# Performance work log

Measured on AMD Instinct MI355X. Metric: run time of the kernel, lower is better.

Reference implementation:

```python
import jax, jax.numpy as jnp
import numpy as np

H = 128; D = 16; L = 4
NP_ = 50000; NL_ = 10000; EPP = 500000; ELP = 100000; EPL = 100000


def _rbf(d):
    # GaussianSmearing(start=0, stop=8, num_gaussians=16)
    off = jnp.linspace(0.0, 8.0, D)
    coeff = -0.5 / ((8.0 / (D - 1)) ** 2)
    x = d[:, None] - off[None, :]
    return jnp.exp(coeff * x * x)


def _layer_norm(x, w, b, eps=1e-5):
    mu = jnp.mean(x, axis=-1, keepdims=True)
    var = jnp.var(x, axis=-1, keepdims=True)
    return (x - mu) * jax.lax.rsqrt(var + eps) * w + b


def _block(x_src, x_dst, src, dst, ea, Wf_, bf_, Ws_, bs_, bnw, bnb, lnw, lnb):
    # CGConv message: z = [x_i(dst), x_j(src), edge_attr]
    z = jnp.concatenate([x_dst[dst], x_src[src], ea], axis=-1)  # [E, 2H+D]
    m = jax.nn.sigmoid(z @ Wf_ + bf_) * jax.nn.softplus(z @ Ws_ + bs_)
    agg = jax.ops.segment_sum(m, dst, num_segments=x_dst.shape[0])
    # BatchNorm1d in eval mode with running_mean=0, running_var=1
    agg = agg * (bnw / jnp.sqrt(1.0 + 1e-5)) + bnb
    out = agg + x_dst            # CGConv internal residual
    out = _layer_norm(out, lnw, lnb)
    out = jax.nn.relu(out)
    return out + x_dst           # ResidualCGConvBlock residual (dropout=identity in eval)


def setup_inputs() -> dict:
    key = jax.random.key(0)
    ks = jax.random.split(key, 16)
    s = lambda n: 1.0 / np.sqrt(n)
    inp = {
        'x_protein': jax.random.normal(ks[0], (NP_, 6), jnp.float32),
        'x_ligand': jax.random.normal(ks[1], (NL_, 6), jnp.float32),
        'ei_pp': jnp.stack([jax.random.randint(ks[2], (EPP,), 0, NP_),
                            jax.random.randint(ks[3], (EPP,), 0, NP_)]).astype(jnp.int32),
        'ea_pp': jax.random.uniform(ks[4], (EPP,), jnp.float32, 0.0, 8.0),
        'ei_lp': jnp.stack([jax.random.randint(ks[5], (ELP,), 0, NL_),
                            jax.random.randint(ks[6], (ELP,), 0, NP_)]).astype(jnp.int32),
        'ea_lp': jax.random.uniform(ks[7], (ELP,), jnp.float32, 0.0, 8.0),
        'ei_pl': jnp.stack([jax.random.randint(ks[8], (EPL,), 0, NP_),
                            jax.random.randint(ks[9], (EPL,), 0, NL_)]).astype(jnp.int32),
        'ea_pl': jax.random.uniform(ks[10], (EPL,), jnp.float32, 0.0, 8.0),
        'Wp': jax.random.normal(ks[11], (6, H), jnp.float32) * s(6),
        'bp': jnp.zeros((H,), jnp.float32),
        'Wl': jax.random.normal(ks[12], (6, H), jnp.float32) * s(6),
        'bl': jnp.zeros((H,), jnp.float32),
        'Wf': jax.random.normal(ks[13], (L, 3, 2 * H + D, H), jnp.float32) * s(2 * H + D),
        'bf': jnp.zeros((L, 3, H), jnp.float32),
        'Ws': jax.random.normal(ks[14], (L, 3, 2 * H + D, H), jnp.float32) * s(2 * H + D),
        'bs': jnp.zeros((L, 3, H), jnp.float32),
        'bn_w': jnp.ones((L, 3, H), jnp.float32),
        'bn_b': jnp.zeros((L, 3, H), jnp.float32),
        'ln_w': jnp.ones((L, 3, H), jnp.float32),
        'ln_b': jnp.zeros((L, 3, H), jnp.float32),
        'lno_w': jnp.ones((H,), jnp.float32),
        'lno_b': jnp.zeros((H,), jnp.float32),
        'fc_w': jax.random.normal(ks[15], (H, 21), jnp.float32) * s(H),
        'fc_b': jnp.zeros((21,), jnp.float32),
    }
    return inp


def reference(x_protein, x_ligand, ei_pp, ea_pp, ei_lp, ea_lp, ei_pl, ea_pl,
              Wp, bp, Wl, bl, Wf, bf, Ws, bs, bn_w, bn_b, ln_w, ln_b,
              lno_w, lno_b, fc_w, fc_b):
    xp = x_protein @ Wp + bp
    xl = x_ligand @ Wl + bl
    rpp = _rbf(ea_pp); rlp = _rbf(ea_lp); rpl = _rbf(ea_pl)
    for l in range(L):
        # HeteroConv aggr='sum': protein receives from pp and lp; ligand from pl
        p_pp = _block(xp, xp, ei_pp[0], ei_pp[1], rpp, Wf[l, 0], bf[l, 0], Ws[l, 0], bs[l, 0],
                      bn_w[l, 0], bn_b[l, 0], ln_w[l, 0], ln_b[l, 0])
        p_lp = _block(xl, xp, ei_lp[0], ei_lp[1], rlp, Wf[l, 1], bf[l, 1], Ws[l, 1], bs[l, 1],
                      bn_w[l, 1], bn_b[l, 1], ln_w[l, 1], ln_b[l, 1])
        l_pl = _block(xp, xl, ei_pl[0], ei_pl[1], rpl, Wf[l, 2], bf[l, 2], Ws[l, 2], bs[l, 2],
                      bn_w[l, 2], bn_b[l, 2], ln_w[l, 2], ln_b[l, 2])
        xp, xl = p_pp + p_lp, l_pl
    out = _layer_norm(xp, lno_w, lno_b)
    return out @ fc_w + fc_b
```

## Files before the change

### kernel.cpp

```cpp
#include <hip/hip_runtime.h>
#include <hip/hip_bf16.h>
#include <math.h>

#define H 128

typedef __bf16 bf16x8 __attribute__((ext_vector_type(8)));
typedef float f32x4 __attribute__((ext_vector_type(4)));
typedef float f32x2 __attribute__((ext_vector_type(2)));
typedef __hip_bfloat16 bf16;
typedef unsigned int uint32;

static __device__ __forceinline__ float bf2f(bf16 v){ return __bfloat162float(v); }
static __device__ __forceinline__ bf16 f2bf(float v){ return __float2bfloat16(v); }
static __device__ __forceinline__ float u2f_lo(uint32 v){ return __uint_as_float(v << 16); }
static __device__ __forceinline__ float u2f_hi(uint32 v){ return __uint_as_float(v & 0xffff0000u); }

union bfpack { struct { bf16 lo, hi; } h; uint32 u; };
static __device__ __forceinline__ uint32 pack_bf2(float a, float b){
  bfpack p; p.h.lo = f2bf(a); p.h.hi = f2bf(b); return p.u;
}

static __device__ __forceinline__ int unperm64(int r){
  int base = r & ~63; int g = r & 63; int t = g >> 4; int j = g & 15;
  return base + 4*j + t;
}

#define NBIN 256
#define PREP_WP_N (4*1024*128)
#define PREP_WL_N (4*512*128)
#define RBF_N     (12*(NBIN+1)*128)

__global__ void prep_all(const float* __restrict__ Wf, const float* __restrict__ Ws,
                         const float* __restrict__ bfv, const float* __restrict__ bsv,
                         bf16* __restrict__ Wt_p, float* __restrict__ Bias_p,
                         bf16* __restrict__ Wt_l, float* __restrict__ Bias_l,
                         bf16* __restrict__ T2,
                         const float* __restrict__ Xp, const float* __restrict__ Wp,
                         const float* __restrict__ bp, float* __restrict__ Xpo,
                         bf16* __restrict__ Xpb, int NP,
                         const float* __restrict__ Xl, const float* __restrict__ Wl,
                         const float* __restrict__ bl, float* __restrict__ Xlo,
                         bf16* __restrict__ Xlb, int NL){
  int t = blockIdx.x*blockDim.x + threadIdx.x;
  if (t < PREP_WP_N){
    int k = t & 127; int idx = t >> 7;
    int rs = idx & 1023; int l = idx >> 10;
    int r = unperm64(rs);
    int rel, c, row0; const float* W; float bias = 0.f;
    if (r < 256)      { rel=0; c=r>>1;        row0=128; W = (r&1)?Ws:Wf; }
    else if (r < 512) { rel=2; c=(r-256)>>1;  row0=128; W = (r&1)?Ws:Wf; }
    else if (r < 640) { rel=0; c=r-512; row0=0; W=Wf; bias = bfv[(l*3+rel)*H+c]; }
    else if (r < 768) { rel=0; c=r-640; row0=0; W=Ws; bias = bsv[(l*3+rel)*H+c]; }
    else if (r < 896) { rel=1; c=r-768; row0=0; W=Wf; bias = bfv[(l*3+rel)*H+c]; }
    else              { rel=1; c=r-896; row0=0; W=Ws; bias = bsv[(l*3+rel)*H+c]; }
    Wt_p[t] = f2bf(W[((size_t)(l*3+rel)*272 + row0 + k)*H + c]);
    if (k == 0) Bias_p[l*1024 + r] = bias;
    return;
  }
  t -= PREP_WP_N;
  if (t < PREP_WL_N){
    int k = t & 127; int idx = t >> 7;
    int rs = idx & 511; int l = idx >> 9;
    int r = unperm64(rs);
    int rel, c, row0; const float* W; float bias = 0.f;
    if (r < 256)      { rel=1; c=r>>1;   row0=128; W = (r&1)?Ws:Wf; }
    else if (r < 384) { rel=2; c=r-256; row0=0; W=Wf; bias = bfv[(l*3+rel)*H+c]; }
    else              { rel=2; c=r-384; row0=0; W=Ws; bias = bsv[(l*3+rel)*H+c]; }
    Wt_l[t] = f2bf(W[((size_t)(l*3+rel)*272 + row0 + k)*H + c]);
    if (k == 0) Bias_l[l*512 + r] = bias;
    return;
  }
  t -= PREP_WL_N;
  if (t < RBF_N){
    int c = t & 127;
    int b = (t >> 7) % (NBIN+1);
    int pr = t / ((NBIN+1)*128);
    float d0 = (float)b * (8.0f/(float)NBIN);
    const float* wf = Wf + ((size_t)pr*272 + 256)*H + c;
    const float* ws = Ws + ((size_t)pr*272 + 256)*H + c;
    float f0=0.f, s0=0.f;
    #pragma unroll
    for (int k=0;k<16;k++){
      float o = 0.533333333f*(float)k;
      float tt = d0 - o;
      float r0 = __expf(-1.7578125f*tt*tt);
      f0 += r0*wf[(size_t)k*H]; s0 += r0*ws[(size_t)k*H];
    }
    bf16* o = T2 + ((size_t)(pr*(NBIN+1) + b))*256 + 2*c;
    o[0]=f2bf(f0); o[1]=f2bf(s0);
    return;
  }
  t -= RBF_N;
  {
    int idx = t;
    const float* Xin; const float* W; const float* b; float* Xout; bf16* Xbf;
    if (idx < NP*H){ Xin=Xp; W=Wp; b=bp; Xout=Xpo; Xbf=Xpb; }
    else { idx -= NP*H; if (idx >= NL*H) return; Xin=Xl; W=Wl; b=bl; Xout=Xlo; Xbf=Xlb; }
    int n = idx >> 7, c = idx & 127;
    float acc = b[c];
    #pragma unroll
    for (int k=0;k<6;k++) acc += Xin[n*6+k] * W[k*H+c];
    Xout[idx] = acc;
    Xbf[idx] = f2bf(acc);
  }
}

__global__ void hist3_k(const int* __restrict__ dpp, int Epp,
                        const int* __restrict__ dlp, int Elp,
                        const int* __restrict__ dpl, int Epl,
                        int* __restrict__ cpp, int* __restrict__ clp, int* __restrict__ cpl){
  int e = blockIdx.x*blockDim.x + threadIdx.x;
  if (e < Epp) atomicAdd(&cpp[dpp[e]], 1);
  else if (e < Epp+Elp) atomicAdd(&clp[dlp[e-Epp]], 1);
  else if (e < Epp+Elp+Epl) atomicAdd(&cpl[dpl[e-Epp-Elp]], 1);
}

#define SCH 1024

__global__ void __launch_bounds__(256) chunksum_k(
    const int* __restrict__ counts, int NP, int NL, int Cpp, int Cpl,
    int* __restrict__ chsum){
  __shared__ int wred[4];
  int b = blockIdx.x;
  const int* cnt; int n; int ch;
  if (b < Cpp){ cnt = counts; n = NP; ch = b; }
  else if (b < 2*Cpp){ cnt = counts + NP; n = NP; ch = b - Cpp; }
  else { cnt = counts + 2*NP; n = NL; ch = b - 2*Cpp; }
  int base = ch * SCH;
  int tid = threadIdx.x;
  int s = 0;
  #pragma unroll
  for (int j=0;j<SCH/256;j++){
    int i = base + tid + j*256;
    if (i < n) s += cnt[i];
  }
  #pragma unroll
  for (int o=32;o>=1;o>>=1) s += __shfl_xor(s,o,64);
  if ((tid & 63) == 0) wred[tid>>6] = s;
  __syncthreads();
  if (tid == 0) chsum[b] = wred[0]+wred[1]+wred[2]+wred[3];
}

__global__ void __launch_bounds__(192) scanmid_k(
    int* __restrict__ chsum, int Cpp, int Cpl, int NP, int NL,
    int* __restrict__ rp_pp, int* __restrict__ rp_lp, int* __restrict__ rp_pl){
  int wid = threadIdx.x >> 6, lane = threadIdx.x & 63;
  int C, off; int* rp_end; int n;
  if (wid == 0){ C = Cpp; off = 0;      rp_end = rp_pp; n = NP; }
  else if (wid == 1){ C = Cpp; off = Cpp; rp_end = rp_lp; n = NP; }
  else { C = Cpl; off = 2*Cpp; rp_end = rp_pl; n = NL; }
  int v = (lane < C) ? chsum[off + lane] : 0;
  int x = v;
  #pragma unroll
  for (int o=1;o<64;o<<=1){
    int y = __shfl_up(x, o, 64);
    if (lane >= o) x += y;
  }
  if (lane < C) chsum[off + lane] = x - v;
  if (lane == 63) rp_end[n] = x;
}

__global__ void __launch_bounds__(1024) scanfin_k(
    const int* __restrict__ counts, int NP, int NL, int Cpp, int Cpl,
    const int* __restrict__ chsum,
    int* __restrict__ rp_pp, int* __restrict__ cur_pp,
    int* __restrict__ rp_lp, int* __restrict__ cur_lp,
    int* __restrict__ rp_pl, int* __restrict__ cur_pl){
  __shared__ int wsum[16];
  int b = blockIdx.x;
  const int* cnt; int n, ch; int* rp; int* cur;
  if (b < Cpp){ cnt = counts; n = NP; ch = b; rp = rp_pp; cur = cur_pp; }
  else if (b < 2*Cpp){ cnt = counts + NP; n = NP; ch = b - Cpp; rp = rp_lp; cur = cur_lp; }
  else { cnt = counts + 2*NP; n = NL; ch = b - 2*Cpp; rp = rp_pl; cur = cur_pl; }
  int tid = threadIdx.x, lane = tid & 63, wid = tid >> 6;
  int i = ch*SCH + tid;
  int v = (i < n) ? cnt[i] : 0;
  int x = v;
  #pragma unroll
  for (int o=1;o<64;o<<=1){
    int y = __shfl_up(x, o, 64);
    if (lane >= o) x += y;
  }
  if (lane == 63) wsum[wid] = x;
  __syncthreads();
  if (wid == 0 && lane < 16){
    int w = wsum[lane];
    #pragma unroll
    for (int o=1;o<16;o<<=1){
      int y = __shfl_up(w, o, 64);
      if (lane >= o) w += y;
    }
    wsum[lane] = w;
  }
  __syncthreads();
  int waveoff = (wid == 0) ? 0 : wsum[wid-1];
  int ex = chsum[b] + waveoff + x - v;
  if (i < n){ rp[i] = ex; cur[i] = ex; }
}

__global__ void fill3_k(const int* __restrict__ ei_pp, const float* __restrict__ ea_pp, int Epp,
                        const int* __restrict__ ei_lp, const float* __restrict__ ea_lp, int Elp,
                        const int* __restrict__ ei_pl, const float* __restrict__ ea_pl, int Epl,
                        int* __restrict__ cur_pp, int2* __restrict__ e2_pp,
                        int* __restrict__ cur_lp, int2* __restrict__ e2_lp,
                        int* __restrict__ cur_pl, int2* __restrict__ e2_pl){
  int e = blockIdx.x*blockDim.x + threadIdx.x;
  if (e < Epp){
    int p = atomicAdd(&cur_pp[ei_pp[Epp + e]], 1);
    e2_pp[p] = make_int2(ei_pp[e], __float_as_int(ea_pp[e]));
  } else if (e < Epp+Elp){
    int i = e - Epp;
    int p = atomicAdd(&cur_lp[ei_lp[Elp + i]], 1);
    e2_lp[p] = make_int2(ei_lp[i], __float_as_int(ea_lp[i]));
  } else if (e < Epp+Elp+Epl){
    int i = e - Epp - Elp;
    int p = atomicAdd(&cur_pl[ei_pl[Epl + i]], 1);
    e2_pl[p] = make_int2(ei_pl[i], __float_as_int(ea_pl[i]));
  }
}

#define GR 8
__global__ void __launch_bounds__(256) gemm_tables(
    const bf16* __restrict__ Xp, const bf16* __restrict__ Wtp,
    const float* __restrict__ Biasp, bf16* __restrict__ Outp,
    int strips_p, int tasks_p,
    const bf16* __restrict__ Xl, const bf16* __restrict__ Wtl,
    const float* __restrict__ Biasl, bf16* __restrict__ Outl,
    int strips_l, int tasks_total){
  int wt = blockIdx.x*4 + (threadIdx.x >> 6);
  if (wt >= tasks_total) return;
  const bf16 *X, *Wt; const float* Bias; bf16* Out; int N, strips, g, chunk;
  if (wt < tasks_p){
    X=Xp; Wt=Wtp; Bias=Biasp; Out=Outp; N=1024; strips=strips_p;
    g = wt & 15; chunk = wt >> 4;
  } else {
    int w = wt - tasks_p;
    X=Xl; Wt=Wtl; Bias=Biasl; Out=Outl; N=512; strips=strips_l;
    g = w & 7; chunk = w >> 3;
  }
  int n0 = g << 6;
  int lane = threadIdx.x & 63;
  int lr = lane & 15, lq = lane >> 4;
  const bf16x8* B0 = (const bf16x8*)(const void*)(Wt + (size_t)(n0      + lr)*H);
  const bf16x8* B1 = (const bf16x8*)(const void*)(Wt + (size_t)(n0 + 16 + lr)*H);
  const bf16x8* B2 = (const bf16x8*)(const void*)(Wt + (size_t)(n0 + 32 + lr)*H);
  const bf16x8* B3 = (const bf16x8*)(const void*)(Wt + (size_t)(n0 + 48 + lr)*H);
  bf16x8 b0_0=B0[lq], b0_1=B0[4+lq], b0_2=B0[8+lq], b0_3=B0[12+lq];
  bf16x8 b1_0=B1[lq], b1_1=B1[4+lq], b1_2=B1[8+lq], b1_3=B1[12+lq];
  bf16x8 b2_0=B2[lq], b2_1=B2[4+lq], b2_2=B2[8+lq], b2_3=B2[12+lq];
  bf16x8 b3_0=B3[lq], b3_1=B3[4+lq], b3_2=B3[8+lq], b3_3=B3[12+lq];
  float4 bias = ((const float4*)(const void*)(Bias + n0))[lr];
  #pragma unroll 2
  for (int r=0;r<GR;r++){
    int strip = chunk*GR + r;
    if (strip >= strips) break;
    int m0 = strip << 4;
    const bf16x8* A = (const bf16x8*)(const void*)(X + (size_t)(m0+lr)*H);
    bf16x8 a0 = A[lq], a1 = A[4+lq], a2 = A[8+lq], a3 = A[12+lq];
    f32x4 acc0 = {0.f,0.f,0.f,0.f}, acc1 = acc0, acc2 = acc0, acc3 = acc0;
    acc0 = __builtin_amdgcn_mfma_f32_16x16x32_bf16(a0, b0_0, acc0, 0, 0, 0);
    acc1 = __builtin_amdgcn_mfma_f32_16x16x32_bf16(a0, b1_0, acc1, 0, 0, 0);
    acc2 = __builtin_amdgcn_mfma_f32_16x16x32_bf16(a0, b2_0, acc2, 0, 0, 0);
    acc3 = __builtin_amdgcn_mfma_f32_16x16x32_bf16(a0, b3_0, acc3, 0, 0, 0);
    acc0 = __builtin_amdgcn_mfma_f32_16x16x32_bf16(a1, b0_1, acc0, 0, 0, 0);
    acc1 = __builtin_amdgcn_mfma_f32_16x16x32_bf16(a1, b1_1, acc1, 0, 0, 0);
    acc2 = __builtin_amdgcn_mfma_f32_16x16x32_bf16(a1, b2_1, acc2, 0, 0, 0);
    acc3 = __builtin_amdgcn_mfma_f32_16x16x32_bf16(a1, b3_1, acc3, 0, 0, 0);
    acc0 = __builtin_amdgcn_mfma_f32_16x16x32_bf16(a2, b0_2, acc0, 0, 0, 0);
    acc1 = __builtin_amdgcn_mfma_f32_16x16x32_bf16(a2, b1_2, acc1, 0, 0, 0);
    acc2 = __builtin_amdgcn_mfma_f32_16x16x32_bf16(a2, b2_2, acc2, 0, 0, 0);
    acc3 = __builtin_amdgcn_mfma_f32_16x16x32_bf16(a2, b3_2, acc3, 0, 0, 0);
    acc0 = __builtin_amdgcn_mfma_f32_16x16x32_bf16(a3, b0_3, acc0, 0, 0, 0);
    acc1 = __builtin_amdgcn_mfma_f32_16x16x32_bf16(a3, b1_3, acc1, 0, 0, 0);
    acc2 = __builtin_amdgcn_mfma_f32_16x16x32_bf16(a3, b2_3, acc2, 0, 0, 0);
    acc3 = __builtin_amdgcn_mfma_f32_16x16x32_bf16(a3, b3_3, acc3, 0, 0, 0);
    #pragma unroll
    for (int rr=0;rr<4;rr++){
      int row = m0 + lq*4 + rr;
      uint2 pk;
      pk.x = pack_bf2(acc0[rr] + bias.x, acc1[rr] + bias.y);
      pk.y = pack_bf2(acc2[rr] + bias.z, acc3[rr] + bias.w);
      *(uint2*)(void*)(Out + (size_t)row*N + n0 + 4*lr) = pk;
    }
  }
}

static __device__ __forceinline__ float act_msg(float f, float s){
  float sig = __builtin_amdgcn_rcpf(1.f + __builtin_amdgcn_exp2f(f * -1.44269504f));
  float e   = __builtin_amdgcn_exp2f(fminf(s, 60.f) * 1.44269504f);
  float sp  = 0.69314718f * __builtin_amdgcn_logf(1.f + e);
  return sig * sp;
}

#define BN_RSQ 0.9999950000374997f

static __device__ __forceinline__ void edge_nb(uint2 g, uint2 t,
                                               f32x2 fd2, f32x2 sd2, f32x2& acc){
  f32x2 f2, s2;
  f2.x = u2f_lo(g.x) + u2f_lo(t.x);
  f2.y = u2f_lo(g.y) + u2f_lo(t.y);
  s2.x = u2f_hi(g.x) + u2f_hi(t.x);
  s2.y = u2f_hi(g.y) + u2f_hi(t.y);
  f2 += fd2; s2 += sd2;
  acc.x += act_msg(f2.x, s2.x);
  acc.y += act_msg(f2.y, s2.y);
}

static __device__ __forceinline__ void ln_stats_w(float v0, float v1, float& mu, float& var){
  float s = v0 + v1, q = v0*v0 + v1*v1;
  #pragma unroll
  for (int o=32;o>=1;o>>=1){ s += __shfl_xor(s,o,64); q += __shfl_xor(q,o,64); }
  mu = s * (1.f/128.f);
  var = q * (1.f/128.f) - mu*mu;
}

static __device__ __forceinline__ void aggregate(
    const int2* __restrict__ ev_arr, int e0, int e1,
    const uint2* __restrict__ G, int gstride, int goff,
    const uint2* __restrict__ Tb, int lane,
    f32x2 fd2, f32x2 sd2, f32x2& acc)
{
  for (int base = e0; base < e1; base += 64){
    int idx = base + lane;
    int2 ev = ev_arr[(idx < e1) ? idx : (e1-1)];
    float dd = __int_as_float(ev.y);
    int bnv = (int)__fmaf_rn(dd, (float)NBIN/8.0f, 0.5f);
    bnv = (bnv > NBIN) ? NBIN : bnv;
    int cnt = e1 - base; cnt = (cnt > 64) ? 64 : cnt;
    uint2 gA, tA, gB, tB, gC, tC;
    #define LDJ(gX, tX, j) { \
      int s_ = __builtin_amdgcn_readlane(ev.x, (j)); \
      int b_ = __builtin_amdgcn_readlane(bnv, (j)); \
      gX = G[(size_t)s_*gstride + goff + lane]; \
      tX = Tb[(size_t)b_*64 + lane]; }
    LDJ(gA, tA, 0);
    if (cnt > 1) LDJ(gB, tB, 1);
    if (cnt > 2) LDJ(gC, tC, 2);
    int j = 0;
    for (; j+5 < cnt; j += 3){
      edge_nb(gA, tA, fd2, sd2, acc); LDJ(gA, tA, j+3);
      edge_nb(gB, tB, fd2, sd2, acc); LDJ(gB, tB, j+4);
      edge_nb(gC, tC, fd2, sd2, acc); LDJ(gC, tC, j+5);
    }
    int rem = cnt - j;
    edge_nb(gA, tA, fd2, sd2, acc);
    if (rem > 3) LDJ(gA, tA, j+3);
    if (rem > 1) edge_nb(gB, tB, fd2, sd2, acc);
    if (rem > 4) LDJ(gB, tB, j+4);
    if (rem > 2) edge_nb(gC, tC, fd2, sd2, acc);
    if (rem > 3) edge_nb(gA, tA, fd2, sd2, acc);
    if (rem > 4) edge_nb(gB, tB, fd2, sd2, acc);
    #undef LDJ
  }
}

__global__ void __launch_bounds__(256) node_update(
    const bf16* __restrict__ PT, const bf16* __restrict__ LT,
    const float* __restrict__ xp, const float* __restrict__ xl,
    const int* __restrict__ pp_rp, const int2* __restrict__ pp_e2,
    const int* __restrict__ lp_rp, const int2* __restrict__ lp_e2,
    const int* __restrict__ pl_rp, const int2* __restrict__ pl_e2,
    const bf16* __restrict__ T2,
    const float* __restrict__ bn_w, const float* __restrict__ bn_b,
    const float* __restrict__ ln_w, const float* __restrict__ ln_b,
    float* __restrict__ xp_out, bf16* __restrict__ xp_bf,
    float* __restrict__ xl_out, bf16* __restrict__ xl_bf,
    int layer, int NP, int NL, int PB)
{
  int wave = threadIdx.x >> 6;
  int lane = threadIdx.x & 63;
  const uint2* PTg = (const uint2*)(const void*)PT;
  if ((int)blockIdx.x < PB){
    int node = blockIdx.x*4 + wave;
    if (node >= NP) return;
    float2 x = ((const float2*)(const void*)(xp + (size_t)node*H))[lane];
    const uint32* PTu = (const uint32*)(const void*)PT;
    const uint2*  LTg = (const uint2*)(const void*)LT;
    float o1_0, o1_1, o2_0, o2_1;
    {
      int pr = layer*3 + 0;
      uint32 fdp = PTu[(size_t)node*512 + 256 + lane];
      uint32 sdp = PTu[(size_t)node*512 + 320 + lane];
      const uint2* Tb = (const uint2*)(const void*)(T2 + (size_t)pr*(NBIN+1)*256);
      f32x2 fd2 = {u2f_lo(fdp), u2f_hi(fdp)};
      f32x2 sd2 = {u2f_lo(sdp), u2f_hi(sdp)};
      f32x2 acc = {0.f, 0.f};
      aggregate(pp_e2, pp_rp[node], pp_rp[node+1], PTg, 256, 0, Tb, lane, fd2, sd2, acc);
      float2 bw = ((const float2*)(const void*)(bn_w + pr*H))[lane];
      float2 bb = ((const float2*)(const void*)(bn_b + pr*H))[lane];
      float2 lw = ((const float2*)(const void*)(ln_w + pr*H))[lane];
      float2 lb = ((const float2*)(const void*)(ln_b + pr*H))[lane];
      float v0 = acc.x * (bw.x * BN_RSQ) + bb.x + x.x;
      float v1 = acc.y * (bw.y * BN_RSQ) + bb.y + x.y;
      float mu, var; ln_stats_w(v0, v1, mu, var);
      float rs = rsqrtf(var + 1e-5f);
      o1_0 = fmaxf((v0-mu)*rs*lw.x + lb.x, 0.f) + x.x;
      o1_1 = fmaxf((v1-mu)*rs*lw.y + lb.y, 0.f) + x.y;
    }
    {
      int pr = layer*3 + 1;
      uint32 fdp = PTu[(size_t)node*512 + 384 + lane];
      uint32 sdp = PTu[(size_t)node*512 + 448 + lane];
      const uint2* Tb = (const uint2*)(const void*)(T2 + (size_t)pr*(NBIN+1)*256);
      f32x2 fd2 = {u2f_lo(fdp), u2f_hi(fdp)};
      f32x2 sd2 = {u2f_lo(sdp), u2f_hi(sdp)};
      f32x2 acc = {0.f, 0.f};
      aggregate(lp_e2, lp_rp[node], lp_rp[node+1], LTg, 128, 0, Tb, lane, fd2, sd2, acc);
      float2 bw = ((const float2*)(const void*)(bn_w + pr*H))[lane];
      float2 bb = ((const float2*)(const void*)(bn_b + pr*H))[lane];
      float2 lw = ((const float2*)(const void*)(ln_w + pr*H))[lane];
      float2 lb = ((const float2*)(const void*)(ln_b + pr*H))[lane];
      float v0 = acc.x * (bw.x * BN_RSQ) + bb.x + x.x;
      float v1 = acc.y * (bw.y * BN_RSQ) + bb.y + x.y;
      float mu, var; ln_stats_w(v0, v1, mu, var);
      float rs = rsqrtf(var + 1e-5f);
      o2_0 = fmaxf((v0-mu)*rs*lw.x + lb.x, 0.f) + x.x;
      o2_1 = fmaxf((v1-mu)*rs*lw.y + lb.y, 0.f) + x.y;
    }
    float out0 = o1_0 + o2_0, out1 = o1_1 + o2_1;
    ((float2*)(void*)(xp_out + (size_t)node*H))[lane] = make_float2(out0, out1);
    ((uint32*)(void*)(xp_bf + (size_t)node*H))[lane] = pack_bf2(out0, out1);
  } else {
    int node = (blockIdx.x - PB)*4 + wave;
    if (node >= NL) return;
    float2 x = ((const float2*)(const void*)(xl + (size_t)node*H))[lane];
    const uint32* LTu = (const uint32*)(const void*)LT;
    int pr = layer*3 + 2;
    uint32 fdp = LTu[(size_t)node*256 + 128 + lane];
    uint32 sdp = LTu[(size_t)node*256 + 192 + lane];
    const uint2* Tb = (const uint2*)(const void*)(T2 + (size_t)pr*(NBIN+1)*256);
    f32x2 fd2 = {u2f_lo(fdp), u2f_hi(fdp)};
    f32x2 sd2 = {u2f_lo(sdp), u2f_hi(sdp)};
    f32x2 acc = {0.f, 0.f};
    aggregate(pl_e2, pl_rp[node], pl_rp[node+1], PTg, 256, 64, Tb, lane, fd2, sd2, acc);
    float2 bw = ((const float2*)(const void*)(bn_w + pr*H))[lane];
    float2 bb = ((const float2*)(const void*)(bn_b + pr*H))[lane];
    float2 lw = ((const float2*)(const void*)(ln_w + pr*H))[lane];
    float2 lb = ((const float2*)(const void*)(ln_b + pr*H))[lane];
    float v0 = acc.x * (bw.x * BN_RSQ) + bb.x + x.x;
    float v1 = acc.y * (bw.y * BN_RSQ) + bb.y + x.y;
    float mu, var; ln_stats_w(v0, v1, mu, var);
    float rs = rsqrtf(var + 1e-5f);
    float out0 = fmaxf((v0-mu)*rs*lw.x + lb.x, 0.f) + x.x;
    float out1 = fmaxf((v1-mu)*rs*lw.y + lb.y, 0.f) + x.y;
    ((float2*)(void*)(xl_out + (size_t)node*H))[lane] = make_float2(out0, out1);
    ((uint32*)(void*)(xl_bf + (size_t)node*H))[lane] = pack_bf2(out0, out1);
  }
}

__global__ void __launch_bounds__(128) final_k(const float* __restrict__ xp,
    const float* __restrict__ lnw, const float* __restrict__ lnb,
    const float* __restrict__ fcw, const float* __restrict__ fcb,
    float* __restrict__ out, int N){
  __shared__ float sm[4];
  __shared__ float lnv[128];
  int node = blockIdx.x, c = threadIdx.x;
  float v = xp[(size_t)node*H + c];
  float s = v, q = v*v;
  #pragma unroll
  for (int o=32;o>=1;o>>=1){ s += __shfl_xor(s,o,64); q += __shfl_xor(q,o,64); }
  __syncthreads();
  if ((c & 63) == 0){ sm[(c>>6)*2] = s; sm[(c>>6)*2+1] = q; }
  __syncthreads();
  float S = sm[0] + sm[2], Q = sm[1] + sm[3];
  float mu = S * (1.f/128.f);
  float var = Q * (1.f/128.f) - mu*mu;
  float ln = (v-mu)*rsqrtf(var+1e-5f)*lnw[c] + lnb[c];
  lnv[c] = ln;
  __syncthreads();
  if (c < 21){
    float a = fcb[c];
    #pragma unroll 4
    for (int i=0;i<128;i++) a += lnv[i]*fcw[i*21+c];
    out[(size_t)node*21 + c] = a;
  }
}

extern "C" void kernel_launch(void* const* d_in, const int* in_sizes, int n_in,
                              void* d_out, int out_size, void* d_ws, size_t ws_size,
                              hipStream_t stream){
  const float* x_protein = (const float*)d_in[0];
  const float* x_ligand  = (const float*)d_in[1];
  const int*   ei_pp = (const int*)d_in[2];
  const float* ea_pp = (const float*)d_in[3];
  const int*   ei_lp = (const int*)d_in[4];
  const float* ea_lp = (const float*)d_in[5];
  const int*   ei_pl = (const int*)d_in[6];
  const float* ea_pl = (const float*)d_in[7];
  const float* Wp  = (const float*)d_in[8];
  const float* bp  = (const float*)d_in[9];
  const float* Wl  = (const float*)d_in[10];
  const float* bl  = (const float*)d_in[11];
  const float* Wf  = (const float*)d_in[12];
  const float* bfv = (const float*)d_in[13];
  const float* Wsv = (const float*)d_in[14];
  const float* bsv = (const float*)d_in[15];
  const float* bn_w = (const float*)d_in[16];
  const float* bn_b = (const float*)d_in[17];
  const float* ln_w = (const float*)d_in[18];
  const float* ln_b = (const float*)d_in[19];
  const float* lno_w = (const float*)d_in[20];
  const float* lno_b = (const float*)d_in[21];
  const float* fc_w = (const float*)d_in[22];
  const float* fc_b = (const float*)d_in[23];

  int NP  = in_sizes[0]/6, NL = in_sizes[1]/6;
  int EPP = in_sizes[3], ELP = in_sizes[5], EPL = in_sizes[7];

  char* ws = (char*)d_ws;
  size_t off = 0;
  auto alloc = [&](size_t bytes)->void*{
    void* p = ws + off; off = (off + bytes + 255) & ~(size_t)255; return p;
  };

  float* xpA = (float*)alloc((size_t)NP*H*4);
  float* xpB = (float*)alloc((size_t)NP*H*4);
  float* xlA = (float*)alloc((size_t)NL*H*4);
  float* xlB = (float*)alloc((size_t)NL*H*4);
  bf16* xp_bf = (bf16*)alloc((size_t)NP*H*2);
  bf16* xl_bf = (bf16*)alloc((size_t)NL*H*2);
  bf16* PT    = (bf16*)alloc((size_t)NP*1024*2);
  bf16* LT    = (bf16*)alloc((size_t)NL*512*2);
  bf16* Wt_p  = (bf16*)alloc((size_t)4*1024*H*2);
  bf16* Wt_l  = (bf16*)alloc((size_t)4*512*H*2);
  float* Bias_p = (float*)alloc((size_t)4*1024*4);
  float* Bias_l = (float*)alloc((size_t)4*512*4);
  bf16* T2    = (bf16*)alloc((size_t)12*(NBIN+1)*256*2);
  int* counts = (int*)alloc((size_t)(2*NP+NL)*4);
  int* rp_pp  = (int*)alloc((size_t)(NP+1)*4);
  int* cur_pp = (int*)alloc((size_t)NP*4);
  int* rp_lp  = (int*)alloc((size_t)(NP+1)*4);
  int* cur_lp = (int*)alloc((size_t)NP*4);
  int* rp_pl  = (int*)alloc((size_t)(NL+1)*4);
  int* cur_pl = (int*)alloc((size_t)NL*4);
  int2* e2_pp = (int2*)alloc((size_t)EPP*8);
  int2* e2_lp = (int2*)alloc((size_t)ELP*8);
  int2* e2_pl = (int2*)alloc((size_t)EPL*8);
  int Cpp = (NP + SCH - 1) / SCH;
  int Cpl = (NL + SCH - 1) / SCH;
  int* chsum = (int*)alloc((size_t)(2*Cpp + Cpl)*4);
  (void)ws_size; (void)n_in; (void)out_size;

  size_t prep_total = (size_t)PREP_WP_N + PREP_WL_N + RBF_N + (size_t)(NP+NL)*H;
  prep_all<<<(prep_total+255)/256, 256, 0, stream>>>(Wf, Wsv, bfv, bsv,
      Wt_p, Bias_p, Wt_l, Bias_l, T2,
      x_protein, Wp, bp, xpA, xp_bf, NP,
      x_ligand,  Wl, bl, xlA, xl_bf, NL);
  hipMemsetAsync(counts, 0, (size_t)(2*NP+NL)*4, stream);
  int* cnt_pp = counts; int* cnt_lp = counts + NP; int* cnt_pl = counts + 2*NP;
  int Etot = EPP + ELP + EPL;
  hist3_k<<<(Etot+255)/256, 256, 0, stream>>>(ei_pp+EPP, EPP, ei_lp+ELP, ELP, ei_pl+EPL, EPL,
                                              cnt_pp, cnt_lp, cnt_pl);
  chunksum_k<<<2*Cpp + Cpl, 256, 0, stream>>>(counts, NP, NL, Cpp, Cpl, chsum);
  scanmid_k<<<1, 192, 0, stream>>>(chsum, Cpp, Cpl, NP, NL, rp_pp, rp_lp, rp_pl);
  scanfin_k<<<2*Cpp + Cpl, 1024, 0, stream>>>(counts, NP, NL, Cpp, Cpl, chsum,
                                              rp_pp, cur_pp, rp_lp, cur_lp, rp_pl, cur_pl);
  fill3_k<<<(Etot+255)/256, 256, 0, stream>>>(ei_pp, ea_pp, EPP, ei_lp, ea_lp, ELP,
                                              ei_pl, ea_pl, EPL,
                                              cur_pp, e2_pp, cur_lp, e2_lp, cur_pl, e2_pl);

  float* xp_cur = xpA; float* xp_nxt = xpB;
  float* xl_cur = xlA; float* xl_nxt = xlB;
  int strips_p = NP >> 4, strips_l = NL >> 4;
  int tasks_p = 16 * ((strips_p + GR - 1) / GR);
  int tasks_l = 8  * ((strips_l + GR - 1) / GR);
  int tasks_total = tasks_p + tasks_l;
  int PB = (NP + 3) / 4, LB = (NL + 3) / 4;
  for (int l=0; l<4; l++){
    gemm_tables<<<(tasks_total+3)/4, 256, 0, stream>>>(
        xp_bf, Wt_p + (size_t)l*1024*H, Bias_p + l*1024, PT, strips_p, tasks_p,
        xl_bf, Wt_l + (size_t)l*512*H,  Bias_l + l*512,  LT, strips_l, tasks_total);
    node_update<<<PB + LB, 256, 0, stream>>>(PT, LT, xp_cur, xl_cur,
        rp_pp, e2_pp, rp_lp, e2_lp, rp_pl, e2_pl, T2,
        bn_w, bn_b, ln_w, ln_b, xp_nxt, xp_bf, xl_nxt, xl_bf, l, NP, NL, PB);
    float* t;
    t = xp_cur; xp_cur = xp_nxt; xp_nxt = t;
    t = xl_cur; xl_cur = xl_nxt; xl_nxt = t;
  }

  final_k<<<NP, 128, 0, stream>>>(xp_cur, lno_w, lno_b, fc_w, fc_b, (float*)d_out, NP);
}
```

Before: 817.4 us.

## Split each node's edge aggregation across two waves with LDS reduction

Result: slower. 870.1 us (+6.4%).

```diff
diff --git a/kernel.cpp b/kernel.cpp
--- a/kernel.cpp
+++ b/kernel.cpp
@@ -365,27 +365,74 @@
     const float* __restrict__ ln_w, const float* __restrict__ ln_b,
     float* __restrict__ xp_out, bf16* __restrict__ xp_bf,
     float* __restrict__ xl_out, bf16* __restrict__ xl_bf,
-    int layer, int NP, int NL, int PB)
+    int layer, int NP, int NL, int PB2)
 {
+  __shared__ float2 lds[512];
   int wave = threadIdx.x >> 6;
   int lane = threadIdx.x & 63;
+  int nib = wave >> 1, pw = wave & 1;
   const uint2* PTg = (const uint2*)(const void*)PT;
-  if ((int)blockIdx.x < PB){
-    int node = blockIdx.x*4 + wave;
-    if (node >= NP) return;
-    float2 x = ((const float2*)(const void*)(xp + (size_t)node*H))[lane];
-    const uint32* PTu = (const uint32*)(const void*)PT;
-    const uint2*  LTg = (const uint2*)(const void*)LT;
-    float o1_0, o1_1, o2_0, o2_1;
-    {
-      int pr = layer*3 + 0;
-      uint32 fdp = PTu[(size_t)node*512 + 256 + lane];
-      uint32 sdp = PTu[(size_t)node*512 + 320 + lane];
+  bool isP = (int)blockIdx.x < PB2;
+  int node = isP ? ((int)blockIdx.x*2 + nib) : (((int)blockIdx.x - PB2)*2 + nib);
+  bool active = isP ? (node < NP) : (node < NL);
+  f32x2 accA = {0.f,0.f};
+  f32x2 accB = {0.f,0.f};
+  float2 x = make_float2(0.f, 0.f);
+  if (active){
+    if (isP){
+      x = ((const float2*)(const void*)(xp + (size_t)node*H))[lane];
+      const uint32* PTu = (const uint32*)(const void*)PT;
+      const uint2*  LTg = (const uint2*)(const void*)LT;
+      {
+        int pr = layer*3 + 0;
+        uint32 fdp = PTu[(size_t)node*512 + 256 + lane];
+        uint32 sdp = PTu[(size_t)node*512 + 320 + lane];
+        const uint2* Tb = (const uint2*)(const void*)(T2 + (size_t)pr*(NBIN+1)*256);
+        f32x2 fd2 = {u2f_lo(fdp), u2f_hi(fdp)};
+        f32x2 sd2 = {u2f_lo(sdp), u2f_hi(sdp)};
+        int e0 = pp_rp[node], e1 = pp_rp[node+1];
+        int h = (e1 - e0 + 1) >> 1;
+        int a0 = e0 + pw*h, a1 = pw ? e1 : (e0 + h);
+        aggregate(pp_e2, a0, a1, PTg, 256, 0, Tb, lane, fd2, sd2, accA);
+      }
+      {
+        int pr = layer*3 + 1;
+        uint32 fdp = PTu[(size_t)node*512 + 384 + lane];
+        uint32 sdp = PTu[(size_t)node*512 + 448 + lane];
+        const uint2* Tb = (const uint2*)(const void*)(T2 + (size_t)pr*(NBIN+1)*256);
+        f32x2 fd2 = {u2f_lo(fdp), u2f_hi(fdp)};
+        f32x2 sd2 = {u2f_lo(sdp), u2f_hi(sdp)};
+        int e0 = lp_rp[node], e1 = lp_rp[node+1];
+        int h = (e1 - e0 + 1) >> 1;
+        int a0 = e0 + pw*h, a1 = pw ? e1 : (e0 + h);
+        aggregate(lp_e2, a0, a1, LTg, 128, 0, Tb, lane, fd2, sd2, accB);
+      }
+    } else {
+      x = ((const float2*)(const void*)(xl + (size_t)node*H))[lane];
+      const uint32* LTu = (const uint32*)(const void*)LT;
+      int pr = layer*3 + 2;
+      uint32 fdp = LTu[(size_t)node*256 + 128 + lane];
+      uint32 sdp = LTu[(size_t)node*256 + 192 + lane];
       const uint2* Tb = (const uint2*)(const void*)(T2 + (size_t)pr*(NBIN+1)*256);
       f32x2 fd2 = {u2f_lo(fdp), u2f_hi(fdp)};
       f32x2 sd2 = {u2f_lo(sdp), u2f_hi(sdp)};
-      f32x2 acc = {0.f, 0.f};
-      aggregate(pp_e2, pp_rp[node], pp_rp[node+1], PTg, 256, 0, Tb, lane, fd2, sd2, acc);
+      int e0 = pl_rp[node], e1 = pl_rp[node+1];
+      int h = (e1 - e0 + 1) >> 1;
+      int a0 = e0 + pw*h, a1 = pw ? e1 : (e0 + h);
+      aggregate(pl_e2, a0, a1, PTg, 256, 64, Tb, lane, fd2, sd2, accA);
+    }
+  }
+  lds[((nib*2 + 0)*2 + pw)*64 + lane] = make_float2(accA.x, accA.y);
+  lds[((nib*2 + 1)*2 + pw)*64 + lane] = make_float2(accB.x, accB.y);
+  __syncthreads();
+  float o0 = 0.f, o1 = 0.f;
+  if (active){
+    if (isP){
+      int rel = pw;
+      float2 partner = lds[((nib*2 + rel)*2 + (1 - pw))*64 + lane];
+      f32x2 acc = (pw == 0) ? accA : accB;
+      acc.x += partner.x; acc.y += partner.y;
+      int pr = layer*3 + rel;
       float2 bw = ((const float2*)(const void*)(bn_w + pr*H))[lane];
       float2 bb = ((const float2*)(const void*)(bn_b + pr*H))[lane];
       float2 lw = ((const float2*)(const void*)(ln_w + pr*H))[lane];
@@ -394,18 +441,14 @@
       float v1 = acc.y * (bw.y * BN_RSQ) + bb.y + x.y;
       float mu, var; ln_stats_w(v0, v1, mu, var);
       float rs = rsqrtf(var + 1e-5f);
-      o1_0 = fmaxf((v0-mu)*rs*lw.x + lb.x, 0.f) + x.x;
-      o1_1 = fmaxf((v1-mu)*rs*lw.y + lb.y, 0.f) + x.y;
-    }
-    {
-      int pr = layer*3 + 1;
-      uint32 fdp = PTu[(size_t)node*512 + 384 + lane];
-      uint32 sdp = PTu[(size_t)node*512 + 448 + lane];
-      const uint2* Tb = (const uint2*)(const void*)(T2 + (size_t)pr*(NBIN+1)*256);
-      f32x2 fd2 = {u2f_lo(fdp), u2f_hi(fdp)};
-      f32x2 sd2 = {u2f_lo(sdp), u2f_hi(sdp)};
-      f32x2 acc = {0.f, 0.f};
-      aggregate(lp_e2, lp_rp[node], lp_rp[node+1], LTg, 128, 0, Tb, lane, fd2, sd2, acc);
+      o0 = fmaxf((v0-mu)*rs*lw.x + lb.x, 0.f) + x.x;
+      o1 = fmaxf((v1-mu)*rs*lw.y + lb.y, 0.f) + x.y;
+      if (pw == 1) lds[((nib*2 + 1)*2 + 1)*64 + lane] = make_float2(o0, o1);
+    } else if (pw == 0){
+      float2 partner = lds[((nib*2 + 0)*2 + 1)*64 + lane];
+      f32x2 acc = accA;
+      acc.x += partner.x; acc.y += partner.y;
+      int pr = layer*3 + 2;
       float2 bw = ((const float2*)(const void*)(bn_w + pr*H))[lane];
       float2 bb = ((const float2*)(const void*)(bn_b + pr*H))[lane];
       float2 lw = ((const float2*)(const void*)(ln_w + pr*H))[lane];
@@ -414,37 +457,18 @@
       float v1 = acc.y * (bw.y * BN_RSQ) + bb.y + x.y;
       float mu, var; ln_stats_w(v0, v1, mu, var);
       float rs = rsqrtf(var + 1e-5f);
-      o2_0 = fmaxf((v0-mu)*rs*lw.x + lb.x, 0.f) + x.x;
-      o2_1 = fmaxf((v1-mu)*rs*lw.y + lb.y, 0.f) + x.y;
+      float out0 = fmaxf((v0-mu)*rs*lw.x + lb.x, 0.f) + x.x;
+      float out1 = fmaxf((v1-mu)*rs*lw.y + lb.y, 0.f) + x.y;
+      ((float2*)(void*)(xl_out + (size_t)node*H))[lane] = make_float2(out0, out1);
+      ((uint32*)(void*)(xl_bf + (size_t)node*H))[lane] = pack_bf2(out0, out1);
     }
-    float out0 = o1_0 + o2_0, out1 = o1_1 + o2_1;
+  }
+  __syncthreads();
+  if (active && isP && pw == 0){
+    float2 o2 = lds[((nib*2 + 1)*2 + 1)*64 + lane];
+    float out0 = o0 + o2.x, out1 = o1 + o2.y;
     ((float2*)(void*)(xp_out + (size_t)node*H))[lane] = make_float2(out0, out1);
     ((uint32*)(void*)(xp_bf + (size_t)node*H))[lane] = pack_bf2(out0, out1);
-  } else {
-    int node = (blockIdx.x - PB)*4 + wave;
-    if (node >= NL) return;
-    float2 x = ((const float2*)(const void*)(xl + (size_t)node*H))[lane];
-    const uint32* LTu = (const uint32*)(const void*)LT;
-    int pr = layer*3 + 2;
-    uint32 fdp = LTu[(size_t)node*256 + 128 + lane];
-    uint32 sdp = LTu[(size_t)node*256 + 192 + lane];
-    const uint2* Tb = (const uint2*)(const void*)(T2 + (size_t)pr*(NBIN+1)*256);
-    f32x2 fd2 = {u2f_lo(fdp), u2f_hi(fdp)};
-    f32x2 sd2 = {u2f_lo(sdp), u2f_hi(sdp)};
-    f32x2 acc = {0.f, 0.f};
-    aggregate(pl_e2, pl_rp[node], pl_rp[node+1], PTg, 256, 64, Tb, lane, fd2, sd2, acc);
-    float2 bw = ((const float2*)(const void*)(bn_w + pr*H))[lane];
-    float2 bb = ((const float2*)(const void*)(bn_b + pr*H))[lane];
-    float2 lw = ((const float2*)(const void*)(ln_w + pr*H))[lane];
-    float2 lb = ((const float2*)(const void*)(ln_b + pr*H))[lane];
-    float v0 = acc.x * (bw.x * BN_RSQ) + bb.x + x.x;
-    float v1 = acc.y * (bw.y * BN_RSQ) + bb.y + x.y;
-    float mu, var; ln_stats_w(v0, v1, mu, var);
-    float rs = rsqrtf(var + 1e-5f);
-    float out0 = fmaxf((v0-mu)*rs*lw.x + lb.x, 0.f) + x.x;
-    float out1 = fmaxf((v1-mu)*rs*lw.y + lb.y, 0.f) + x.y;
-    ((float2*)(void*)(xl_out + (size_t)node*H))[lane] = make_float2(out0, out1);
-    ((uint32*)(void*)(xl_bf + (size_t)node*H))[lane] = pack_bf2(out0, out1);
   }
 }
 
@@ -565,14 +589,14 @@
   int tasks_p = 16 * ((strips_p + GR - 1) / GR);
   int tasks_l = 8  * ((strips_l + GR - 1) / GR);
   int tasks_total = tasks_p + tasks_l;
-  int PB = (NP + 3) / 4, LB = (NL + 3) / 4;
+  int PB2 = (NP + 1) / 2, LB2 = (NL + 1) / 2;
   for (int l=0; l<4; l++){
     gemm_tables<<<(tasks_total+3)/4, 256, 0, stream>>>(
         xp_bf, Wt_p + (size_t)l*1024*H, Bias_p + l*1024, PT, strips_p, tasks_p,
         xl_bf, Wt_l + (size_t)l*512*H,  Bias_l + l*512,  LT, strips_l, tasks_total);
-    node_update<<<PB + LB, 256, 0, stream>>>(PT, LT, xp_cur, xl_cur,
+    node_update<<<PB2 + LB2, 256, 0, stream>>>(PT, LT, xp_cur, xl_cur,
         rp_pp, e2_pp, rp_lp, e2_lp, rp_pl, e2_pl, T2,
-        bn_w, bn_b, ln_w, ln_b, xp_nxt, xp_bf, xl_nxt, xl_bf, l, NP, NL, PB);
+        bn_w, bn_b, ln_w, ln_b, xp_nxt, xp_bf, xl_nxt, xl_bf, l, NP, NL, PB2);
     float* t;
     t = xp_cur; xp_cur = xp_nxt; xp_nxt = t;
     t = xl_cur; xl_cur = xl_nxt; xl_nxt = t;
```
